# Performance work log

Measured on AMD Instinct MI355X. Metric: run time of the kernel, lower is better.

Reference implementation:

```python
import jax, jax.numpy as jnp
import numpy as np

N_USERS = 100000
N_ITEMS = 100000
D_FEAT = 256
BATCH = 8192
CLASSES = 5
E = 500000
D_CONV = 128
D_RAW = 256
D_EMB = 256
NUM_BASIS = 2
BN_EPS = 1e-3  # tf.contrib.layers.batch_norm default epsilon


def _bn_params(key, dim):
    # packed [gamma, beta, moving_mean, moving_var]
    return jnp.stack([jnp.ones(dim), jnp.zeros(dim), jnp.zeros(dim), jnp.ones(dim)]).astype(jnp.float32)


def setup_inputs() -> dict:
    key = jax.random.key(0)
    ks = jax.random.split(key, 24)
    s = lambda fan_in, fan_out: np.sqrt(2.0 / (fan_in + fan_out)).astype(np.float32)
    inp = {
        'user_feat': jax.random.normal(ks[0], (N_USERS, D_FEAT), jnp.float32),
        'item_feat': jax.random.normal(ks[1], (N_ITEMS, D_FEAT), jnp.float32),
        'user_idx': jax.random.randint(ks[2], (BATCH,), 0, N_USERS, jnp.int32),
        'item_idx': jax.random.randint(ks[3], (BATCH,), 0, N_ITEMS, jnp.int32),
        'user_edge_src': jax.random.randint(ks[4], (CLASSES, E), 0, N_ITEMS, jnp.int32),
        'user_edge_dst': jax.random.randint(ks[5], (CLASSES, E), 0, BATCH, jnp.int32),
        'user_edge_w': jax.random.uniform(ks[6], (CLASSES, E), jnp.float32),
        'item_edge_src': jax.random.randint(ks[7], (CLASSES, E), 0, N_USERS, jnp.int32),
        'item_edge_dst': jax.random.randint(ks[8], (CLASSES, E), 0, BATCH, jnp.int32),
        'item_edge_w': jax.random.uniform(ks[9], (CLASSES, E), jnp.float32),
        'W_fu': jax.random.normal(ks[10], (D_FEAT, D_RAW), jnp.float32) * s(D_FEAT, D_RAW),
        'b_fu': jnp.zeros((D_RAW,), jnp.float32),
        'W_fi': jax.random.normal(ks[11], (D_FEAT, D_RAW), jnp.float32) * s(D_FEAT, D_RAW),
        'b_fi': jnp.zeros((D_RAW,), jnp.float32),
        'W_uc': jax.random.normal(ks[12], (CLASSES, D_FEAT, D_CONV), jnp.float32) * s(D_FEAT, D_CONV),
        'W_ic': jax.random.normal(ks[13], (CLASSES, D_FEAT, D_CONV), jnp.float32) * s(D_FEAT, D_CONV),
        'bn_fu': _bn_params(ks[14], D_RAW),
        'bn_hu': _bn_params(ks[15], CLASSES * D_CONV),
        'bn_fi': _bn_params(ks[16], D_RAW),
        'bn_hi': _bn_params(ks[17], CLASSES * D_CONV),
        'W2_fu': jax.random.normal(ks[18], (D_RAW, D_EMB), jnp.float32) * s(D_RAW, D_EMB),
        'W2_hu': jax.random.normal(ks[19], (CLASSES * D_CONV, D_EMB), jnp.float32) * s(CLASSES * D_CONV, D_EMB),
        'W2_fi': jax.random.normal(ks[20], (D_RAW, D_EMB), jnp.float32) * s(D_RAW, D_EMB),
        'W2_hi': jax.random.normal(ks[21], (CLASSES * D_CONV, D_EMB), jnp.float32) * s(CLASSES * D_CONV, D_EMB),
        'Wdec': jax.random.normal(ks[22], (NUM_BASIS, D_EMB, D_EMB), jnp.float32) * s(D_EMB, D_EMB),
        'Wcomb': jax.random.normal(ks[23], (CLASSES, NUM_BASIS), jnp.float32) * s(CLASSES, NUM_BASIS),
    }
    return inp


def _bn(x, p):
    gamma, beta, mean, var = p[0], p[1], p[2], p[3]
    return gamma * (x - mean) * jax.lax.rsqrt(var + BN_EPS) + beta


def _agg(feat, src, dst, w, n_rows):
    # weighted sparse [B, N] x dense [N, D] aggregation via gather + segment_sum
    msgs = feat[src] * w[:, None]  # [E, D]
    return jax.ops.segment_sum(msgs, dst, num_segments=n_rows)


def reference(user_feat, item_feat, user_idx, item_idx,
              user_edge_src, user_edge_dst, user_edge_w,
              item_edge_src, item_edge_dst, item_edge_w,
              W_fu, b_fu, W_fi, b_fi, W_uc, W_ic,
              bn_fu, bn_hu, bn_fi, bn_hi,
              W2_fu, W2_hu, W2_fi, W2_hi, Wdec, Wcomb):
    B = user_idx.shape[0]
    classes = W_uc.shape[0]

    # batch row selection (sparse.matmul with one-hot selector == gather)
    f_user = user_feat[user_idx] @ W_fu + b_fu  # [B, D_RAW]
    f_item = item_feat[item_idx] @ W_fi + b_fi

    # per-class graph convolution: aggregate opposite-side features, project, stack
    h_user = jnp.concatenate(
        [_agg(item_feat, user_edge_src[c], user_edge_dst[c], user_edge_w[c], B) @ W_uc[c]
         for c in range(classes)], axis=1)  # [B, classes*D_CONV]
    h_item = jnp.concatenate(
        [_agg(user_feat, item_edge_src[c], item_edge_dst[c], item_edge_w[c], B) @ W_ic[c]
         for c in range(classes)], axis=1)

    # batchnorm (inference stats) + relu  (dropout rate 0 -> identity)
    f_user = jax.nn.relu(_bn(f_user, bn_fu))
    f_item = jax.nn.relu(_bn(f_item, bn_fi))
    h_user = jax.nn.relu(_bn(h_user, bn_hu))
    h_item = jax.nn.relu(_bn(h_item, bn_hi))

    user_emb = jax.nn.relu(f_user @ W2_fu + h_user @ W2_hu)  # [B, D_EMB]
    item_emb = jax.nn.relu(f_item @ W2_fi + h_item @ W2_hi)

    # bilinear decoder: per-class kernel = sum_k Wcomb[r,k] * Wdec[k]
    kernels = jnp.einsum('rk,kij->rij', Wcomb, Wdec)  # [classes, D_EMB, D_EMB]
    logits = jnp.einsum('bi,rij,bj->br', user_emb, kernels, item_emb)  # [B, classes]
    return logits


if __name__ == '__main__':
    out = reference(**setup_inputs())
    print(out.shape, out.dtype)
```

## Files before the change

### kernel.cpp

```cpp
#include <hip/hip_runtime.h>
#include <cstdint>
#include <cstddef>

#define NBATCH   8192
#define DFEAT    256
#define DCONV    128
#define NCLASS   5
#define NEDGE    500000
#define NUSERS   100000
#define BN_EPS   1e-3f
#define NBUCKET  128
#define BROWS    64
#define CAP      4608

typedef unsigned short u16;
typedef short bf16x8_t __attribute__((ext_vector_type(8)));
typedef float f32x4_t  __attribute__((ext_vector_type(4)));

__device__ __forceinline__ u16 f2bf(float x) {
    unsigned u = __float_as_uint(x);
    u += 0x7FFF + ((u >> 16) & 1);
    return (u16)(u >> 16);
}
__device__ __forceinline__ float bf2f(u16 h) {
    return __uint_as_float(((unsigned)h) << 16);
}

__device__ __forceinline__ void mfma_tiles(
    const u16* __restrict__ A, int lda, const int* __restrict__ gather,
    const u16* __restrict__ BT, int K,
    int tileM, int tileN, u16* As, u16* Bs, f32x4_t acc[4])
{
    const int t    = threadIdx.x;
    const int rowi = t >> 2;
    const int kc   = t & 3;
    const int w    = t >> 6;
    const int lane = t & 63;

    int ar = gather ? gather[tileM + rowi] : (tileM + rowi);
    const u16* Ap = A  + (size_t)ar * lda + kc * 8;
    const u16* Bp = BT + (size_t)(tileN + rowi) * K + kc * 8;
    u16* Aw = As + (size_t)(((rowi >> 4) * 64) + (rowi & 15) + 16 * kc) * 8;
    u16* Bw = Bs + (size_t)(((rowi >> 4) * 64) + (rowi & 15) + 16 * kc) * 8;
    const u16* Ar = As + (size_t)(w * 64 + lane) * 8;

    for (int k0 = 0; k0 < K; k0 += 32) {
        __syncthreads();
        *(uint4*)Aw = *(const uint4*)(Ap + k0);
        *(uint4*)Bw = *(const uint4*)(Bp + k0);
        __syncthreads();
        bf16x8_t av = *(const bf16x8_t*)Ar;
        #pragma unroll
        for (int nb = 0; nb < 4; ++nb) {
            bf16x8_t bv = *(const bf16x8_t*)(Bs + (size_t)(nb * 64 + lane) * 8);
            acc[nb] = __builtin_amdgcn_mfma_f32_16x16x32_bf16(av, bv, acc[nb], 0, 0, 0);
        }
    }
}

__device__ __forceinline__ void epilogue(
    f32x4_t acc[4], int tileM, int tileN,
    const float* __restrict__ bias, const float* __restrict__ bn, int bn_ld,
    int relu, u16* __restrict__ out_bf, float* __restrict__ out_f32, int ldc)
{
    const int t = threadIdx.x, w = t >> 6, lane = t & 63;
    const int row0 = tileM + w * 16 + (lane >> 4) * 4;
    #pragma unroll
    for (int nb = 0; nb < 4; ++nb) {
        int col = tileN + nb * 16 + (lane & 15);
        float g = 1.f, be = 0.f, mu = 0.f, va = 1.f, bs = 0.f;
        if (bn)   { g = bn[col]; be = bn[bn_ld + col]; mu = bn[2 * bn_ld + col]; va = bn[3 * bn_ld + col]; }
        if (bias) bs = bias[col];
        #pragma unroll
        for (int r = 0; r < 4; ++r) {
            float x = acc[nb][r] + bs;
            if (bn)   x = g * (x - mu) * rsqrtf(va + BN_EPS) + be;
            if (relu) x = fmaxf(x, 0.f);
            size_t o = (size_t)(row0 + r) * ldc + col;
            if (out_bf) out_bf[o] = f2bf(x);
            else        out_f32[o] = x;
        }
    }
}

__global__ __launch_bounds__(256) void k_gemm_f(
    const u16* __restrict__ ubf, const u16* __restrict__ ibf,
    const int* __restrict__ uidx, const int* __restrict__ iidx,
    const u16* __restrict__ WTu, const u16* __restrict__ WTi,
    const float* __restrict__ bu, const float* __restrict__ bi,
    const float* __restrict__ bnu, const float* __restrict__ bni,
    u16* __restrict__ outu, u16* __restrict__ outi)
{
    __shared__ __align__(16) u16 As[2048], Bs[2048];
    f32x4_t z4 = {0.f, 0.f, 0.f, 0.f};
    f32x4_t acc[4] = {z4, z4, z4, z4};
    int z = blockIdx.z;
    const u16* feat = z ? ibf : ubf;
    const int* idx  = z ? iidx : uidx;
    const u16* WT   = z ? WTi : WTu;
    const float* bias = z ? bi : bu;
    const float* bn   = z ? bni : bnu;
    u16* out = z ? outi : outu;
    int tileM = blockIdx.x * 64, tileN = blockIdx.y * 64;
    mfma_tiles(feat, 256, idx, WT, 256, tileM, tileN, As, Bs, acc);
    epilogue(acc, tileM, tileN, bias, bn, 256, 1, out, nullptr, 256);
}

__global__ __launch_bounds__(256) void k_hproj(
    const u16* __restrict__ agg, const u16* __restrict__ WucT, const u16* __restrict__ WicT,
    const float* __restrict__ bn_hu, const float* __restrict__ bn_hi,
    u16* __restrict__ h_user, u16* __restrict__ h_item)
{
    __shared__ __align__(16) u16 As[2048], Bs[2048];
    f32x4_t z4 = {0.f, 0.f, 0.f, 0.f};
    f32x4_t acc[4] = {z4, z4, z4, z4};
    int cs = blockIdx.z, c = cs % NCLASS, side = cs / NCLASS;
    const u16* A  = agg + (size_t)cs * NBATCH * DFEAT;
    const u16* BT = (side ? WicT : WucT) + (size_t)c * DCONV * DFEAT;
    const float* bn = (side ? bn_hi : bn_hu) + c * DCONV;
    u16* out = (side ? h_item : h_user) + c * DCONV;
    int tileM = blockIdx.x * 64, tileN = blockIdx.y * 64;
    mfma_tiles(A, 256, nullptr, BT, 256, tileM, tileN, As, Bs, acc);
    epilogue(acc, tileM, tileN, nullptr, bn, NCLASS * DCONV, 1, out, nullptr, NCLASS * DCONV);
}

__global__ __launch_bounds__(256) void k_emb(
    const u16* __restrict__ fu, const u16* __restrict__ fi,
    const u16* __restrict__ hu, const u16* __restrict__ hi,
    const u16* __restrict__ W2fTu, const u16* __restrict__ W2hTu,
    const u16* __restrict__ W2fTi, const u16* __restrict__ W2hTi,
    u16* __restrict__ embu, u16* __restrict__ embi)
{
    __shared__ __align__(16) u16 As[2048], Bs[2048];
    f32x4_t z4 = {0.f, 0.f, 0.f, 0.f};
    f32x4_t acc[4] = {z4, z4, z4, z4};
    int z = blockIdx.z;
    const u16* fbf  = z ? fi : fu;
    const u16* hbf  = z ? hi : hu;
    const u16* W2fT = z ? W2fTi : W2fTu;
    const u16* W2hT = z ? W2hTi : W2hTu;
    u16* emb = z ? embi : embu;
    int tileM = blockIdx.x * 64, tileN = blockIdx.y * 64;
    mfma_tiles(fbf, 256, nullptr, W2fT, 256, tileM, tileN, As, Bs, acc);
    mfma_tiles(hbf, NCLASS * DCONV, nullptr, W2hT, NCLASS * DCONV, tileM, tileN, As, Bs, acc);
    epilogue(acc, tileM, tileN, nullptr, nullptr, 0, 1, emb, nullptr, 256);
}

__global__ __launch_bounds__(256) void k_dec(
    const u16* __restrict__ emb, const u16* __restrict__ WdecT,
    float* __restrict__ t0, float* __restrict__ t1)
{
    __shared__ __align__(16) u16 As[2048], Bs[2048];
    f32x4_t z4 = {0.f, 0.f, 0.f, 0.f};
    f32x4_t acc[4] = {z4, z4, z4, z4};
    int zi = blockIdx.z;
    const u16* BT = WdecT + (size_t)zi * 256 * 256;
    float* out = zi ? t1 : t0;
    int tileM = blockIdx.x * 64, tileN = blockIdx.y * 64;
    mfma_tiles(emb, 256, nullptr, BT, 256, tileM, tileN, As, Bs, acc);
    epilogue(acc, tileM, tileN, nullptr, nullptr, 0, 0, nullptr, out, 256);
}

__global__ __launch_bounds__(256) void cvt_feat(
    const float* __restrict__ uf, const float* __restrict__ itf,
    u16* __restrict__ ubf, u16* __restrict__ ibf)
{
    const size_t n4 = (size_t)NUSERS * DFEAT / 4;
    for (size_t i = (size_t)blockIdx.x * 256 + threadIdx.x; i < 2 * n4;
         i += (size_t)gridDim.x * 256) {
        bool u = i < n4;
        size_t j = u ? i : i - n4;
        float4 v = u ? ((const float4*)uf)[j] : ((const float4*)itf)[j];
        ushort4 o;
        o.x = f2bf(v.x); o.y = f2bf(v.y); o.z = f2bf(v.z); o.w = f2bf(v.w);
        ((ushort4*)(u ? ubf : ibf))[j] = o;
    }
}

#define OFF_WFU   0
#define OFF_WFI   65536
#define OFF_WUC   131072
#define OFF_WIC   294912
#define OFF_W2FU  458752
#define OFF_W2HU  524288
#define OFF_W2FI  688128
#define OFF_W2HI  753664
#define OFF_WDEC  917504

__global__ __launch_bounds__(256) void cvt_wt(
    const float* __restrict__ Wfu, const float* __restrict__ Wfi,
    const float* __restrict__ Wuc, const float* __restrict__ Wic,
    const float* __restrict__ W2fu, const float* __restrict__ W2hu,
    const float* __restrict__ W2fi, const float* __restrict__ W2hi,
    const float* __restrict__ Wdec, u16* __restrict__ wT)
{
    const float* in; u16* out; int K, N, B;
    switch (blockIdx.y) {
        case 0: in = Wfu;  out = wT + OFF_WFU;  K = 256; N = 256; B = 1; break;
        case 1: in = Wfi;  out = wT + OFF_WFI;  K = 256; N = 256; B = 1; break;
        case 2: in = Wuc;  out = wT + OFF_WUC;  K = 256; N = 128; B = 5; break;
        case 3: in = Wic;  out = wT + OFF_WIC;  K = 256; N = 128; B = 5; break;
        case 4: in = W2fu; out = wT + OFF_W2FU; K = 256; N = 256; B = 1; break;
        case 5: in = W2hu; out = wT + OFF_W2HU; K = 640; N = 256; B = 1; break;
        case 6: in = W2fi; out = wT + OFF_W2FI; K = 256; N = 256; B = 1; break;
        case 7: in = W2hi; out = wT + OFF_W2HI; K = 640; N = 256; B = 1; break;
        default: in = Wdec; out = wT + OFF_WDEC; K = 256; N = 256; B = 2; break;
    }
    int total = B * K * N;
    for (int idx = blockIdx.x * 256 + threadIdx.x; idx < total; idx += gridDim.x * 256) {
        int b = idx / (K * N);
        int r = idx - b * K * N;
        int n = r / K;
        int k = r - n * K;
        out[idx] = f2bf(in[(size_t)(b * K + k) * N + n]);
    }
}

__global__ __launch_bounds__(256) void init_bcur(int* __restrict__ bcur)
{
    int i = blockIdx.x * 256 + threadIdx.x;
    if (i < 10 * NBUCKET) bcur[i] = (i & (NBUCKET - 1)) * CAP;
}

__global__ __launch_bounds__(256) void partition_kernel(
    const int* __restrict__ u_src, const int* __restrict__ u_dst, const float* __restrict__ u_w,
    const int* __restrict__ i_src, const int* __restrict__ i_dst, const float* __restrict__ i_w,
    int* __restrict__ bcur, uint2* __restrict__ part)
{
    __shared__ int hist[NBUCKET];
    __shared__ int cur[NBUCKET];
    int cs = blockIdx.y;
    const int* srcp; const int* dstp; const float* wp;
    if (cs < NCLASS) {
        srcp = u_src + (size_t)cs * NEDGE;
        dstp = u_dst + (size_t)cs * NEDGE;
        wp   = u_w   + (size_t)cs * NEDGE;
    } else {
        int c = cs - NCLASS;
        srcp = i_src + (size_t)c * NEDGE;
        dstp = i_dst + (size_t)c * NEDGE;
        wp   = i_w   + (size_t)c * NEDGE;
    }
    int lo_e = (int)(((long long)blockIdx.x * NEDGE) / gridDim.x);
    int hi_e = (int)(((long long)(blockIdx.x + 1) * NEDGE) / gridDim.x);

    for (int i = threadIdx.x; i < NBUCKET; i += 256) hist[i] = 0;
    __syncthreads();
    for (int e = lo_e + threadIdx.x; e < hi_e; e += 256)
        atomicAdd(&hist[dstp[e] >> 6], 1);
    __syncthreads();
    for (int i = threadIdx.x; i < NBUCKET; i += 256)
        cur[i] = atomicAdd(&bcur[cs * NBUCKET + i], hist[i]);
    __syncthreads();
    uint2* out = part + (size_t)cs * NBUCKET * CAP;
    for (int e = lo_e + threadIdx.x; e < hi_e; e += 256) {
        int dst = dstp[e];
        int bkt = dst >> 6;
        int pos = atomicAdd(&cur[bkt], 1);
        if (pos < bkt * CAP + CAP)
            out[pos] = make_uint2((unsigned)srcp[e] | ((unsigned)(dst & 63) << 24),
                                  __float_as_uint(wp[e]));
    }
}

__global__ __launch_bounds__(512) void spmm_sorted(
    const u16* __restrict__ item_bf, const u16* __restrict__ user_bf,
    const uint2* __restrict__ part, const int* __restrict__ bcur,
    u16* __restrict__ agg)
{
    __shared__ int bin_cnt[BROWS];
    __shared__ int bin_off[BROWS + 1];
    __shared__ int bin_cur[BROWS];
    __shared__ __align__(8) uint2 sorted[CAP];
    int b  = blockIdx.x;
    int cs = blockIdx.y;
    const u16* feat = (cs < NCLASS) ? item_bf : user_bf;
    int n = bcur[cs * NBUCKET + b] - b * CAP;
    if (n > CAP) n = CAP;
    const uint2* ew = part + ((size_t)cs * NBUCKET + b) * CAP;
    int tid = threadIdx.x, wave = tid >> 6, lane = tid & 63;

    if (tid < BROWS) bin_cnt[tid] = 0;
    __syncthreads();
    for (int e = tid; e < n; e += 512)
        atomicAdd(&bin_cnt[ew[e].x >> 24], 1);
    __syncthreads();
    if (tid < 64) {
        int c = bin_cnt[tid];
        int v = c;
        #pragma unroll
        for (int o = 1; o < 64; o <<= 1) {
            int u = __shfl_up(v, o);
            if (lane >= o) v += u;
        }
        bin_off[tid + 1] = v;
        bin_cur[tid] = v - c;
        if (tid == 0) bin_off[0] = 0;
    }
    __syncthreads();
    for (int e = tid; e < n; e += 512) {
        uint2 p = ew[e];
        int pos = atomicAdd(&bin_cur[p.x >> 24], 1);
        sorted[pos] = p;
    }
    __syncthreads();

    int rowbase = cs * NBATCH + b * BROWS;
    #pragma unroll
    for (int r0 = 0; r0 < 8; ++r0) {
        int r = wave * 8 + r0;
        int j0 = bin_off[r], j1 = bin_off[r + 1];
        float ax = 0.f, ay = 0.f, az = 0.f, aw = 0.f;
        int j = j0;
        for (; j + 7 < j1; j += 8) {
            uint2 p[8];
            #pragma unroll
            for (int q = 0; q < 8; ++q) p[q] = sorted[j + q];
            ushort4 v[8];
            #pragma unroll
            for (int q = 0; q < 8; ++q)
                v[q] = *(const ushort4*)&feat[(size_t)(p[q].x & 0xFFFFFF) * DFEAT + lane * 4];
            #pragma unroll
            for (int q = 0; q < 8; ++q) {
                float w = __uint_as_float(p[q].y);
                ax += w * bf2f(v[q].x);
                ay += w * bf2f(v[q].y);
                az += w * bf2f(v[q].z);
                aw += w * bf2f(v[q].w);
            }
        }
        for (; j + 3 < j1; j += 4) {
            uint2 p0 = sorted[j], p1 = sorted[j + 1], p2 = sorted[j + 2], p3 = sorted[j + 3];
            ushort4 v0 = *(const ushort4*)&feat[(size_t)(p0.x & 0xFFFFFF) * DFEAT + lane * 4];
            ushort4 v1 = *(const ushort4*)&feat[(size_t)(p1.x & 0xFFFFFF) * DFEAT + lane * 4];
            ushort4 v2 = *(const ushort4*)&feat[(size_t)(p2.x & 0xFFFFFF) * DFEAT + lane * 4];
            ushort4 v3 = *(const ushort4*)&feat[(size_t)(p3.x & 0xFFFFFF) * DFEAT + lane * 4];
            float w0 = __uint_as_float(p0.y), w1 = __uint_as_float(p1.y);
            float w2 = __uint_as_float(p2.y), w3 = __uint_as_float(p3.y);
            ax += w0 * bf2f(v0.x) + w1 * bf2f(v1.x) + w2 * bf2f(v2.x) + w3 * bf2f(v3.x);
            ay += w0 * bf2f(v0.y) + w1 * bf2f(v1.y) + w2 * bf2f(v2.y) + w3 * bf2f(v3.y);
            az += w0 * bf2f(v0.z) + w1 * bf2f(v1.z) + w2 * bf2f(v2.z) + w3 * bf2f(v3.z);
            aw += w0 * bf2f(v0.w) + w1 * bf2f(v1.w) + w2 * bf2f(v2.w) + w3 * bf2f(v3.w);
        }
        for (; j < j1; ++j) {
            uint2 p0 = sorted[j];
            ushort4 v0 = *(const ushort4*)&feat[(size_t)(p0.x & 0xFFFFFF) * DFEAT + lane * 4];
            float w0 = __uint_as_float(p0.y);
            ax += w0 * bf2f(v0.x);
            ay += w0 * bf2f(v0.y);
            az += w0 * bf2f(v0.z);
            aw += w0 * bf2f(v0.w);
        }
        ushort4 o4;
        o4.x = f2bf(ax); o4.y = f2bf(ay); o4.z = f2bf(az); o4.w = f2bf(aw);
        *(ushort4*)&agg[(size_t)(rowbase + r) * 256 + lane * 4] = o4;
    }
}

__global__ __launch_bounds__(256) void decoder_kernel(
    const float* __restrict__ t0, const float* __restrict__ t1,
    const u16* __restrict__ item_emb, const float* __restrict__ Wcomb,
    float* __restrict__ out)
{
    int wave = threadIdx.x >> 6;
    int lane = threadIdx.x & 63;
    int b = blockIdx.x * 4 + wave;
    const u16*   ie = item_emb + (size_t)b * 256;
    const float* p0 = t0 + (size_t)b * 256;
    const float* p1 = t1 + (size_t)b * 256;
    float s0 = 0.f, s1 = 0.f;
    #pragma unroll
    for (int j = lane; j < 256; j += 64) {
        float v = bf2f(ie[j]);
        s0 += p0[j] * v;
        s1 += p1[j] * v;
    }
    #pragma unroll
    for (int o = 32; o > 0; o >>= 1) {
        s0 += __shfl_down(s0, o);
        s1 += __shfl_down(s1, o);
    }
    if (lane == 0) {
        #pragma unroll
        for (int r = 0; r < NCLASS; ++r)
            out[b * NCLASS + r] = Wcomb[r * 2 + 0] * s0 + Wcomb[r * 2 + 1] * s1;
    }
}

extern "C" void kernel_launch(void* const* d_in, const int* in_sizes, int n_in,
                              void* d_out, int out_size, void* d_ws, size_t ws_size,
                              hipStream_t stream)
{
    const float* user_feat = (const float*)d_in[0];
    const float* item_feat = (const float*)d_in[1];
    const int*   user_idx  = (const int*)  d_in[2];
    const int*   item_idx  = (const int*)  d_in[3];
    const int*   u_src     = (const int*)  d_in[4];
    const int*   u_dst     = (const int*)  d_in[5];
    const float* u_w       = (const float*)d_in[6];
    const int*   i_src     = (const int*)  d_in[7];
    const int*   i_dst     = (const int*)  d_in[8];
    const float* i_w       = (const float*)d_in[9];
    const float* W_fu      = (const float*)d_in[10];
    const float* b_fu      = (const float*)d_in[11];
    const float* W_fi      = (const float*)d_in[12];
    const float* b_fi      = (const float*)d_in[13];
    const float* W_uc      = (const float*)d_in[14];
    const float* W_ic      = (const float*)d_in[15];
    const float* bn_fu     = (const float*)d_in[16];
    const float* bn_hu     = (const float*)d_in[17];
    const float* bn_fi     = (const float*)d_in[18];
    const float* bn_hi     = (const float*)d_in[19];
    const float* W2_fu     = (const float*)d_in[20];
    const float* W2_hu     = (const float*)d_in[21];
    const float* W2_fi     = (const float*)d_in[22];
    const float* W2_hi     = (const float*)d_in[23];
    const float* Wdec      = (const float*)d_in[24];
    const float* Wcomb     = (const float*)d_in[25];
    float* out = (float*)d_out;

    char* ws = (char*)d_ws;
    int*   bcur       = (int*)  (ws + 0);
    uint2* part_ew    = (uint2*)(ws + 65536);
    u16*   user_bf    = (u16*)  (ws + 47251456);
    u16*   item_bf    = (u16*)  (ws + 98451456);
    u16*   agg_bf     = (u16*)  (ws + 149651456);
    u16*   wT         = (u16*)  (ws + 191594496);
    u16*   f_user_bf  = (u16*)  (ws + 65536);
    u16*   f_item_bf  = (u16*)  (ws + 4259840);
    u16*   h_user_bf  = (u16*)  (ws + 8454144);
    u16*   h_item_bf  = (u16*)  (ws + 18939904);
    float* t0         = (float*)(ws + 149651456);
    float* t1         = (float*)(ws + 158040064);
    u16*   user_emb   = (u16*)  (ws + 166428672);
    u16*   item_emb   = (u16*)  (ws + 170622976);

    init_bcur<<<5, 256, 0, stream>>>(bcur);
    partition_kernel<<<dim3(128, 10), 256, 0, stream>>>(
        u_src, u_dst, u_w, i_src, i_dst, i_w, bcur, part_ew);

    cvt_feat<<<4096, 256, 0, stream>>>(user_feat, item_feat, user_bf, item_bf);
    cvt_wt<<<dim3(160, 9), 256, 0, stream>>>(W_fu, W_fi, W_uc, W_ic,
                                             W2_fu, W2_hu, W2_fi, W2_hi, Wdec, wT);

    spmm_sorted<<<dim3(NBUCKET, 10), 512, 0, stream>>>(
        item_bf, user_bf, part_ew, bcur, agg_bf);

    k_gemm_f<<<dim3(128, 4, 2), 256, 0, stream>>>(
        user_bf, item_bf, user_idx, item_idx, wT + OFF_WFU, wT + OFF_WFI,
        b_fu, b_fi, bn_fu, bn_fi, f_user_bf, f_item_bf);

    k_hproj<<<dim3(128, 2, 10), 256, 0, stream>>>(agg_bf, wT + OFF_WUC, wT + OFF_WIC,
                                                  bn_hu, bn_hi, h_user_bf, h_item_bf);

    k_emb<<<dim3(128, 4, 2), 256, 0, stream>>>(
        f_user_bf, f_item_bf, h_user_bf, h_item_bf,
        wT + OFF_W2FU, wT + OFF_W2HU, wT + OFF_W2FI, wT + OFF_W2HI,
        user_emb, item_emb);

    k_dec<<<dim3(128, 4, 2), 256, 0, stream>>>(user_emb, wT + OFF_WDEC, t0, t1);
    decoder_kernel<<<NBATCH / 4, 256, 0, stream>>>(t0, t1, item_emb, Wcomb, out);
}
```

Measured before the change: 794.1 us.

## Bin edges by source-index phase so concurrent blocks gather from a shared window

The per-bucket edge sort now keys on the destination row combined with a coarse source-index range (eight phases of 16K rows). The gather loop runs phase by phase across all eight rows a wave owns, keeping 32 accumulators live, so blocks tend to touch the same 16K-row slice of the feature table at about the same time. The aim is better L2/MALL hit rates on the random feature gathers. In exchange it adds a two-level block-wide scan over 512 bins, more register pressure and more short inner loops with poorer unrolling.

```diff
diff --git a/kernel.cpp b/kernel.cpp
--- a/kernel.cpp
+++ b/kernel.cpp
@@ -12,6 +12,7 @@
 #define NBUCKET  128
 #define BROWS    64
 #define CAP      4608
+#define NPH      8
 
 typedef unsigned short u16;
 typedef short bf16x8_t __attribute__((ext_vector_type(8)));
@@ -263,14 +264,19 @@
     }
 }
 
+__device__ __forceinline__ int edge_key(unsigned x) {
+    return (int)((x >> 24) * NPH) + (int)(((x & 0xFFFFFF) >> 14) & (NPH - 1));
+}
+
 __global__ __launch_bounds__(512) void spmm_sorted(
     const u16* __restrict__ item_bf, const u16* __restrict__ user_bf,
     const uint2* __restrict__ part, const int* __restrict__ bcur,
     u16* __restrict__ agg)
 {
-    __shared__ int bin_cnt[BROWS];
-    __shared__ int bin_off[BROWS + 1];
-    __shared__ int bin_cur[BROWS];
+    __shared__ int bin_cnt[BROWS * NPH];
+    __shared__ int bin_off[BROWS * NPH + 1];
+    __shared__ int bin_cur[BROWS * NPH];
+    __shared__ int wsum[8];
     __shared__ __align__(8) uint2 sorted[CAP];
     int b  = blockIdx.x;
     int cs = blockIdx.y;
@@ -280,12 +286,12 @@
     const uint2* ew = part + ((size_t)cs * NBUCKET + b) * CAP;
     int tid = threadIdx.x, wave = tid >> 6, lane = tid & 63;
 
-    if (tid < BROWS) bin_cnt[tid] = 0;
+    bin_cnt[tid] = 0;
     __syncthreads();
     for (int e = tid; e < n; e += 512)
-        atomicAdd(&bin_cnt[ew[e].x >> 24], 1);
-    __syncthreads();
-    if (tid < 64) {
+        atomicAdd(&bin_cnt[edge_key(ew[e].x)], 1);
+    __syncthreads();
+    {
         int c = bin_cnt[tid];
         int v = c;
         #pragma unroll
@@ -293,67 +299,90 @@
             int u = __shfl_up(v, o);
             if (lane >= o) v += u;
         }
-        bin_off[tid + 1] = v;
-        bin_cur[tid] = v - c;
+        if (lane == 63) wsum[wave] = v;
+        __syncthreads();
+        if (tid < 8) {
+            int s = wsum[tid];
+            #pragma unroll
+            for (int o = 1; o < 8; o <<= 1) {
+                int u = __shfl_up(s, o);
+                if (lane >= o) s += u;
+            }
+            wsum[tid] = s;
+        }
+        __syncthreads();
+        int base = wave ? wsum[wave - 1] : 0;
+        int incl = v + base;
+        bin_off[tid + 1] = incl;
+        bin_cur[tid] = incl - c;
         if (tid == 0) bin_off[0] = 0;
     }
     __syncthreads();
     for (int e = tid; e < n; e += 512) {
         uint2 p = ew[e];
-        int pos = atomicAdd(&bin_cur[p.x >> 24], 1);
+        int pos = atomicAdd(&bin_cur[edge_key(p.x)], 1);
         sorted[pos] = p;
     }
     __syncthreads();
 
     int rowbase = cs * NBATCH + b * BROWS;
+    float ax[8], ay[8], az[8], aw[8];
+    #pragma unroll
+    for (int r0 = 0; r0 < 8; ++r0) { ax[r0] = 0.f; ay[r0] = 0.f; az[r0] = 0.f; aw[r0] = 0.f; }
+
+    for (int ph = 0; ph < NPH; ++ph) {
+        #pragma unroll
+        for (int r0 = 0; r0 < 8; ++r0) {
+            int bi = (wave * 8 + r0) * NPH + ph;
+            int j0 = bin_off[bi], j1 = bin_off[bi + 1];
+            int j = j0;
+            for (; j + 7 < j1; j += 8) {
+                uint2 p[8];
+                #pragma unroll
+                for (int q = 0; q < 8; ++q) p[q] = sorted[j + q];
+                ushort4 v[8];
+                #pragma unroll
+                for (int q = 0; q < 8; ++q)
+                    v[q] = *(const ushort4*)&feat[(size_t)(p[q].x & 0xFFFFFF) * DFEAT + lane * 4];
+                #pragma unroll
+                for (int q = 0; q < 8; ++q) {
+                    float w = __uint_as_float(p[q].y);
+                    ax[r0] += w * bf2f(v[q].x);
+                    ay[r0] += w * bf2f(v[q].y);
+                    az[r0] += w * bf2f(v[q].z);
+                    aw[r0] += w * bf2f(v[q].w);
+                }
+            }
+            for (; j + 3 < j1; j += 4) {
+                uint2 p0 = sorted[j], p1 = sorted[j + 1], p2 = sorted[j + 2], p3 = sorted[j + 3];
+                ushort4 v0 = *(const ushort4*)&feat[(size_t)(p0.x & 0xFFFFFF) * DFEAT + lane * 4];
+                ushort4 v1 = *(const ushort4*)&feat[(size_t)(p1.x & 0xFFFFFF) * DFEAT + lane * 4];
+                ushort4 v2 = *(const ushort4*)&feat[(size_t)(p2.x & 0xFFFFFF) * DFEAT + lane * 4];
+                ushort4 v3 = *(const ushort4*)&feat[(size_t)(p3.x & 0xFFFFFF) * DFEAT + lane * 4];
+                float w0 = __uint_as_float(p0.y), w1 = __uint_as_float(p1.y);
+                float w2 = __uint_as_float(p2.y), w3 = __uint_as_float(p3.y);
+                ax[r0] += w0 * bf2f(v0.x) + w1 * bf2f(v1.x) + w2 * bf2f(v2.x) + w3 * bf2f(v3.x);
+                ay[r0] += w0 * bf2f(v0.y) + w1 * bf2f(v1.y) + w2 * bf2f(v2.y) + w3 * bf2f(v3.y);
+                az[r0] += w0 * bf2f(v0.z) + w1 * bf2f(v1.z) + w2 * bf2f(v2.z) + w3 * bf2f(v3.z);
+                aw[r0] += w0 * bf2f(v0.w) + w1 * bf2f(v1.w) + w2 * bf2f(v2.w) + w3 * bf2f(v3.w);
+            }
+            for (; j < j1; ++j) {
+                uint2 p0 = sorted[j];
+                ushort4 v0 = *(const ushort4*)&feat[(size_t)(p0.x & 0xFFFFFF) * DFEAT + lane * 4];
+                float w0 = __uint_as_float(p0.y);
+                ax[r0] += w0 * bf2f(v0.x);
+                ay[r0] += w0 * bf2f(v0.y);
+                az[r0] += w0 * bf2f(v0.z);
+                aw[r0] += w0 * bf2f(v0.w);
+            }
+        }
+    }
+
     #pragma unroll
     for (int r0 = 0; r0 < 8; ++r0) {
-        int r = wave * 8 + r0;
-        int j0 = bin_off[r], j1 = bin_off[r + 1];
-        float ax = 0.f, ay = 0.f, az = 0.f, aw = 0.f;
-        int j = j0;
-        for (; j + 7 < j1; j += 8) {
-            uint2 p[8];
-            #pragma unroll
-            for (int q = 0; q < 8; ++q) p[q] = sorted[j + q];
-            ushort4 v[8];
-            #pragma unroll
-            for (int q = 0; q < 8; ++q)
-                v[q] = *(const ushort4*)&feat[(size_t)(p[q].x & 0xFFFFFF) * DFEAT + lane * 4];
-            #pragma unroll
-            for (int q = 0; q < 8; ++q) {
-                float w = __uint_as_float(p[q].y);
-                ax += w * bf2f(v[q].x);
-                ay += w * bf2f(v[q].y);
-                az += w * bf2f(v[q].z);
-                aw += w * bf2f(v[q].w);
-            }
-        }
-        for (; j + 3 < j1; j += 4) {
-            uint2 p0 = sorted[j], p1 = sorted[j + 1], p2 = sorted[j + 2], p3 = sorted[j + 3];
-            ushort4 v0 = *(const ushort4*)&feat[(size_t)(p0.x & 0xFFFFFF) * DFEAT + lane * 4];
-            ushort4 v1 = *(const ushort4*)&feat[(size_t)(p1.x & 0xFFFFFF) * DFEAT + lane * 4];
-            ushort4 v2 = *(const ushort4*)&feat[(size_t)(p2.x & 0xFFFFFF) * DFEAT + lane * 4];
-            ushort4 v3 = *(const ushort4*)&feat[(size_t)(p3.x & 0xFFFFFF) * DFEAT + lane * 4];
-            float w0 = __uint_as_float(p0.y), w1 = __uint_as_float(p1.y);
-            float w2 = __uint_as_float(p2.y), w3 = __uint_as_float(p3.y);
-            ax += w0 * bf2f(v0.x) + w1 * bf2f(v1.x) + w2 * bf2f(v2.x) + w3 * bf2f(v3.x);
-            ay += w0 * bf2f(v0.y) + w1 * bf2f(v1.y) + w2 * bf2f(v2.y) + w3 * bf2f(v3.y);
-            az += w0 * bf2f(v0.z) + w1 * bf2f(v1.z) + w2 * bf2f(v2.z) + w3 * bf2f(v3.z);
-            aw += w0 * bf2f(v0.w) + w1 * bf2f(v1.w) + w2 * bf2f(v2.w) + w3 * bf2f(v3.w);
-        }
-        for (; j < j1; ++j) {
-            uint2 p0 = sorted[j];
-            ushort4 v0 = *(const ushort4*)&feat[(size_t)(p0.x & 0xFFFFFF) * DFEAT + lane * 4];
-            float w0 = __uint_as_float(p0.y);
-            ax += w0 * bf2f(v0.x);
-            ay += w0 * bf2f(v0.y);
-            az += w0 * bf2f(v0.z);
-            aw += w0 * bf2f(v0.w);
-        }
         ushort4 o4;
-        o4.x = f2bf(ax); o4.y = f2bf(ay); o4.z = f2bf(az); o4.w = f2bf(aw);
-        *(ushort4*)&agg[(size_t)(rowbase + r) * 256 + lane * 4] = o4;
+        o4.x = f2bf(ax[r0]); o4.y = f2bf(ay[r0]); o4.z = f2bf(az[r0]); o4.w = f2bf(aw[r0]);
+        *(ushort4*)&agg[(size_t)(rowbase + wave * 8 + r0) * 256 + lane * 4] = o4;
     }
 }
 
```

After: 739.7 us. 6.8% less time.
